# Kernel tuning notes

Measured on AMD Instinct MI355X. Metric: run time of the kernel, lower is better.

The kernel has to match this reference:

```python
import jax, jax.numpy as jnp
import numpy as np
from jax import lax

DIM = 1024
INNER = 2048  # dim * expand_factor
STATE = 64
B, T = 4, 2048
DECAY = 0.95
INPUT_FACTOR = 0.05
LN_EPS = 1e-5


def setup_inputs() -> dict:
    key = jax.random.key(0)
    ks = jax.random.split(key, 8)
    s = 0.02  # small weight scale
    return {
        "x": jax.random.normal(ks[0], (B, T, DIM), jnp.float32),
        "W_in": jax.random.normal(ks[1], (2 * INNER, DIM), jnp.float32) * s,
        "conv_w": jax.random.normal(ks[2], (INNER, 1, 4), jnp.float32) * s,
        "conv_b": jax.random.normal(ks[3], (INNER,), jnp.float32) * s,
        "W_B": jax.random.normal(ks[4], (STATE, INNER), jnp.float32) * s,
        "W_C": jax.random.normal(ks[5], (INNER, STATE), jnp.float32) * s,
        "D_param": jax.random.normal(ks[6], (INNER,), jnp.float32) * s,
        "W_out": jax.random.normal(ks[7], (DIM, INNER), jnp.float32) * s,
        "ln_gamma": jnp.ones((DIM,), jnp.float32),
        "ln_beta": jnp.zeros((DIM,), jnp.float32),
    }


def _layernorm(x, g, b):
    mu = jnp.mean(x, axis=-1, keepdims=True)
    var = jnp.mean(jnp.square(x - mu), axis=-1, keepdims=True)
    return (x - mu) * lax.rsqrt(var + LN_EPS) * g + b


def reference(x, W_in, conv_w, conv_b, W_B, W_C, D_param, W_out, ln_gamma, ln_beta):
    Bn, Tn, Dn = x.shape
    # in_proj -> split into input/gate halves
    x_proj = jnp.einsum("btd,ed->bte", x, W_in)  # [B,T,2*INNER]
    x_input, x_gate = jnp.split(x_proj, 2, axis=-1)
    # depthwise causal conv1d (torch pad=3 then slice [:T] == left-pad 3)
    xc = lax.conv_general_dilated(
        x_input.transpose(0, 2, 1),  # [B,C,T]
        conv_w,                       # [C,1,4]
        window_strides=(1,),
        padding=[(3, 0)],
        feature_group_count=INNER,
    ) + conv_b[None, :, None]
    u = jax.nn.silu(xc).transpose(0, 2, 1)  # [B,T,INNER]
    # linear recurrence: h_t = 0.95*h_{t-1} + 0.05*B_proj(u_t); h_0 = 0
    Bu = jnp.einsum("btc,sc->bts", u, W_B)  # [B,T,STATE]

    def step(h, bu_t):
        h = DECAY * h + INPUT_FACTOR * bu_t
        return h, h

    h0 = jnp.zeros((Bn, STATE), x.dtype)
    _, hs = lax.scan(step, h0, Bu.transpose(1, 0, 2))  # hs: [T,B,STATE]
    hs = hs.transpose(1, 0, 2)  # [B,T,STATE]
    y = jnp.einsum("bts,cs->btc", hs, W_C) + D_param * u  # [B,T,INNER]
    y = y * jax.nn.silu(x_gate)
    y = jnp.einsum("btc,dc->btd", y, W_out)  # [B,T,DIM]
    return _layernorm(y + x, ln_gamma, ln_beta)
```

## Files before the change

kernel.cpp:

```cpp
#include <hip/hip_runtime.h>
#include <hip/hip_bf16.h>

#define T_SEQ 2048
#define DIMD  1024
#define INNER 2048
#define STATE 64
#define BATCH 4
#define NCHUNK 64
#define CHUNK_L (T_SEQ / NCHUNK)
#define MROWS (BATCH * T_SEQ)
#define PSTRIDE ((long)MROWS * STATE)

typedef __hip_bfloat16 bf16;
typedef __attribute__((ext_vector_type(8))) short bf16x8v;
typedef __attribute__((ext_vector_type(4))) float f32x4v;
typedef __attribute__((ext_vector_type(4))) short short4v;

__device__ __forceinline__ float b2f(short s) {
    unsigned u = ((unsigned)(unsigned short)s) << 16;
    float f;
    __builtin_memcpy(&f, &u, 4);
    return f;
}
__device__ __forceinline__ short f2b(float f) {
    bf16 h = __float2bfloat16(f);
    short s;
    __builtin_memcpy(&s, &h, 2);
    return s;
}

__device__ __forceinline__ void gld_lds16(void* lds, const void* gsrc) {
    __builtin_amdgcn_global_load_lds(
        (const __attribute__((address_space(1))) unsigned*)gsrc,
        (__attribute__((address_space(3))) unsigned*)lds, 16, 0, 0);
}

template<int N> __device__ __forceinline__ void waitcnt_vm() {
    if constexpr (N == 8)       asm volatile("s_waitcnt vmcnt(8)" ::: "memory");
    else if constexpr (N == 4)  asm volatile("s_waitcnt vmcnt(4)" ::: "memory");
    else if constexpr (N == 2)  asm volatile("s_waitcnt vmcnt(2)" ::: "memory");
    else                        asm volatile("s_waitcnt vmcnt(0)" ::: "memory");
}
__device__ __forceinline__ void block_barrier() {
    asm volatile("" ::: "memory");
    __builtin_amdgcn_s_barrier();
    asm volatile("" ::: "memory");
}

template<int XSWZ>
__device__ __forceinline__ void swz_block(int& bx, int& by) {
    if constexpr (XSWZ == 1) {
        const int gx = gridDim.x;
        const int nwg = gx * gridDim.y;
        int id = by * gx + bx;
        const int cpx = nwg >> 3;
        id = (id & 7) * cpx + (id >> 3);
        bx = id % gx; by = id / gx;
    } else if constexpr (XSWZ == 2) {
        const int gx = gridDim.x;
        const int gy = gridDim.y;
        const int id = by * gx + bx;
        const int xcd = id & 7;
        const int c   = id >> 3;
        const int rowsX = gy >> 3;
        const int rw  = gx >> 2;
        const int r   = c >> 4;
        const int pos = c & 15;
        const int rbx = (r % rw) << 2;
        const int rby = (r / rw) << 2;
        bx = rbx + (pos & 3);
        by = xcd * rowsX + rby + (pos >> 2);
    }
}

template<int EPI, int XSWZ>
__global__ __launch_bounds__(512, 2)
void gemm_8ph(const short* __restrict__ A, const short* __restrict__ B,
              void* __restrict__ Cout, int M, int N, int K)
{
    __shared__ __align__(16) short As[2][2][128 * 64];
    __shared__ __align__(16) short Bs[2][2][128 * 64];

    int bx = blockIdx.x, by = blockIdx.y;
    swz_block<XSWZ>(bx, by);

    const int tid  = threadIdx.x;
    const int lane = tid & 63;
    const int wave = tid >> 6;
    const int wm2 = (wave >> 2) & 1;
    const int wn2 = wave & 3;
    const long bm = (long)by * 256;
    const long bn = (long)bx * 256;

    const int rsel = lane & 15;
    const int ssrc = (((tid & 7) ^ ((tid >> 3) & 7)) * 8);
    const int swz  = lane & 7;

    f32x4v acc[4][4][2];
#pragma unroll
    for (int q = 0; q < 4; q++)
#pragma unroll
        for (int m = 0; m < 4; m++)
#pragma unroll
            for (int n = 0; n < 2; n++)
                acc[q][m][n] = (f32x4v){0.f, 0.f, 0.f, 0.f};

    const int nt = K / 64;

    auto stage_half = [&](int tt, int h) {
        const int buf = tt & 1;
        const int half = h >> 1;
        const int k0 = tt * 64;
#pragma unroll
        for (int i = 0; i < 2; i++) {
            const int j = i * 512 + tid;
            if (h & 1)
                gld_lds16(&Bs[buf][half][j * 8],
                          &B[(bn + half * 128 + (j >> 3)) * (long)K + k0 + ssrc]);
            else
                gld_lds16(&As[buf][half][j * 8],
                          &A[(bm + half * 128 + (j >> 3)) * (long)K + k0 + ssrc]);
        }
    };

    stage_half(0, 0); stage_half(0, 1); stage_half(0, 2); stage_half(0, 3);
    waitcnt_vm<4>();
    block_barrier();

    for (int t = 0; t < nt; ++t) {
        const int buf = t & 1;
        const bool pf = (t + 1 < nt);
#pragma unroll
        for (int h = 0; h < 4; ++h) {
            const int QM[4] = {0, 1, 1, 0};
            const int QN[4] = {0, 0, 1, 1};
            const int qm = QM[h], qn = QN[h];
            bf16x8v af[4][2], bfv[2][2];
#pragma unroll
            for (int kkh = 0; kkh < 2; kkh++) {
                const int slog = kkh * 4 + (lane >> 4);
                const int soff = ((slog ^ swz) * 8);
#pragma unroll
                for (int m = 0; m < 4; m++) {
                    const int ar = wm2 * 64 + m * 16 + rsel;
                    af[m][kkh] = *(const bf16x8v*)&As[buf][qm][ar * 64 + soff];
                }
#pragma unroll
                for (int n = 0; n < 2; n++) {
                    const int br = wn2 * 32 + n * 16 + rsel;
                    bfv[n][kkh] = *(const bf16x8v*)&Bs[buf][qn][br * 64 + soff];
                }
            }
            if (pf) stage_half(t + 1, h);
            if (pf) {
                if (h == 0) waitcnt_vm<4>();
                else if (h == 1) waitcnt_vm<4>();
                else if (h == 3) waitcnt_vm<4>();
            } else {
                if (h == 0) waitcnt_vm<2>();
                else if (h == 1) waitcnt_vm<0>();
            }
            block_barrier();
            asm volatile("s_waitcnt lgkmcnt(0)" ::: "memory");
            __builtin_amdgcn_sched_barrier(0);
            __builtin_amdgcn_s_setprio(1);
#pragma unroll
            for (int kkh = 0; kkh < 2; kkh++)
#pragma unroll
                for (int m = 0; m < 4; m++)
#pragma unroll
                    for (int n = 0; n < 2; n++)
                        acc[h][m][n] = __builtin_amdgcn_mfma_f32_16x16x32_bf16(
                            af[m][kkh], bfv[n][kkh], acc[h][m][n], 0, 0, 0);
            __builtin_amdgcn_s_setprio(0);
            block_barrier();
        }
    }

#pragma unroll
    for (int q = 0; q < 4; q++) {
        const int QM[4] = {0, 1, 1, 0};
        const int QN[4] = {0, 0, 1, 1};
#pragma unroll
        for (int m = 0; m < 4; m++) {
#pragma unroll
            for (int n = 0; n < 2; n++) {
                const long col  = bn + QN[q] * 128 + wn2 * 32 + n * 16 + (lane & 15);
                const long row0 = bm + QM[q] * 128 + wm2 * 64 + m * 16 + (lane >> 4) * 4;
#pragma unroll
                for (int j = 0; j < 4; j++) {
                    const long idx = (row0 + j) * (long)N + col;
                    ((short*)Cout)[idx] = f2b(acc[q][m][n][j]);
                }
            }
        }
    }
}

template<int BM, int BN, int BK, int WR, int WC, int EPI, int SPLITK, int XSWZ>
__global__ __launch_bounds__(WR*WC*64, 2)
void gemm_ring(const short* __restrict__ A, const short* __restrict__ B,
               void* __restrict__ Cout, int M, int N, int K,
               const short* __restrict__ u_ptr)
{
    constexpr int MFR = BM / (WR * 16);
    constexpr int NFR = BN / (WC * 16);
    constexpr int THREADS = WR * WC * 64;
    constexpr int UPR = BK / 8;
    constexpr int AISS = (BM * UPR) / THREADS;
    constexpr int BISS = (BN * UPR) / THREADS;
    constexpr int LPS  = AISS + BISS;
    __shared__ __align__(16) short As[2][BM * BK];
    __shared__ __align__(16) short Bs[2][BN * BK];

    int bx = blockIdx.x, by = blockIdx.y;
    swz_block<XSWZ>(bx, by);

    const int tid  = threadIdx.x;
    const int lane = tid & 63;
    const int wave = tid >> 6;
    const int wm = (wave / WC) * (MFR * 16);
    const int wn = (wave % WC) * (NFR * 16);
    const long bm = (long)by * BM;
    const long bn = (long)bx * BN;

    f32x4v acc[MFR][NFR];
#pragma unroll
    for (int m = 0; m < MFR; m++)
#pragma unroll
        for (int n = 0; n < NFR; n++)
            acc[m][n] = (f32x4v){0.f, 0.f, 0.f, 0.f};

    const int rsel = lane & 15;
    const int ssrc = (((tid & 7) ^ ((tid >> 3) & 7)) * 8);
    const int swz  = lane & 7;

    int kbeg = 0, kend = K;
    if constexpr (SPLITK > 1) {
        const int kch = K / SPLITK;
        kbeg = blockIdx.z * kch;
        kend = kbeg + kch;
    }
    const int nt = (kend - kbeg) / BK;

    auto stage = [&](int buf, int k0) {
#pragma unroll
        for (int i = 0; i < AISS; i++) {
            const int j = i * THREADS + tid;
            gld_lds16(&As[buf][j * 8],
                      &A[(bm + (j >> 3)) * (long)K + k0 + ssrc]);
        }
#pragma unroll
        for (int i = 0; i < BISS; i++) {
            const int j = i * THREADS + tid;
            gld_lds16(&Bs[buf][j * 8],
                      &B[(bn + (j >> 3)) * (long)K + k0 + ssrc]);
        }
    };
    auto compute = [&](int buf) {
#pragma unroll
        for (int kk = 0; kk < BK; kk += 32) {
            const int slog = (kk >> 3) + (lane >> 4);
            const int soff = ((slog ^ swz) * 8);
            bf16x8v af[MFR], bfv[NFR];
#pragma unroll
            for (int m = 0; m < MFR; m++)
                af[m] = *(const bf16x8v*)&As[buf][(wm + m * 16 + rsel) * BK + soff];
#pragma unroll
            for (int n = 0; n < NFR; n++)
                bfv[n] = *(const bf16x8v*)&Bs[buf][(wn + n * 16 + rsel) * BK + soff];
#pragma unroll
            for (int m = 0; m < MFR; m++)
#pragma unroll
                for (int n = 0; n < NFR; n++)
                    acc[m][n] = __builtin_amdgcn_mfma_f32_16x16x32_bf16(
                        af[m], bfv[n], acc[m][n], 0, 0, 0);
        }
    };

    stage(0, kbeg);
    for (int t = 0; t < nt; ++t) {
        const bool pf = (t + 1 < nt);
        if (pf) stage((t + 1) & 1, kbeg + (t + 1) * BK);
        if (pf) waitcnt_vm<LPS>();
        else    waitcnt_vm<0>();
        block_barrier();
        compute(t & 1);
        block_barrier();
    }

    float* fout = (float*)Cout;
    if constexpr (SPLITK > 1)
        fout += (long)blockIdx.z * (long)M * N;

#pragma unroll
    for (int m = 0; m < MFR; m++) {
#pragma unroll
        for (int n = 0; n < NFR; n++) {
            const long col  = bn + wn + n * 16 + (lane & 15);
            const long row0 = bm + wm + m * 16 + (lane >> 4) * 4;
#pragma unroll
            for (int j = 0; j < 4; j++) {
                const long row = row0 + j;
                const float v = acc[m][n][j];
                const long idx = row * (long)N + col;
                if constexpr (EPI == 0) {
                    ((short*)Cout)[idx] = f2b(v);
                } else if constexpr (EPI == 1) {
                    fout[idx] = v;
                } else {
                    ((short*)Cout)[idx] = f2b(v + b2f(u_ptr[idx]));
                }
            }
        }
    }
}

__global__ __launch_bounds__(256)
void conv_silu_kernel(const short* __restrict__ xproj, const float* __restrict__ cw,
                      const float* __restrict__ cb, short* __restrict__ u)
{
    const int bt = blockIdx.x;
    const int t  = bt & (T_SEQ - 1);
    const int c0 = threadIdx.x * 8;

    float wreg[4][8];
#pragma unroll
    for (int i = 0; i < 8; i++) {
        float4 wv = *(const float4*)&cw[(c0 + i) * 4];
        wreg[0][i] = wv.x; wreg[1][i] = wv.y; wreg[2][i] = wv.z; wreg[3][i] = wv.w;
    }
    float acc[8];
#pragma unroll
    for (int i = 0; i < 8; i++) acc[i] = cb[c0 + i];

#pragma unroll
    for (int k = 0; k < 4; k++) {
        if (t - 3 + k < 0) continue;
        bf16x8v v = *(const bf16x8v*)&xproj[(long)(bt - 3 + k) * (2 * INNER) + c0];
#pragma unroll
        for (int i = 0; i < 8; i++) acc[i] += b2f(v[i]) * wreg[k][i];
    }
    short o[8];
#pragma unroll
    for (int i = 0; i < 8; i++) {
        float s = acc[i] / (1.f + __expf(-acc[i]));
        o[i] = f2b(s);
    }
    *(bf16x8v*)&u[(long)bt * INNER + c0] = *(const bf16x8v*)o;
}

#define EBS 132
__global__ __launch_bounds__(256, 2)
void gemm3_fused(const short* __restrict__ hs, const short* __restrict__ Wc,
                 short* __restrict__ yg, const short* __restrict__ gate_ptr,
                 const float* __restrict__ Dp)
{
    __shared__ __align__(16) short As[128 * 64];
    __shared__ __align__(16) short Bs[128 * 64];
    __shared__ __align__(16) float eb[64 * EBS];

    const int tid  = threadIdx.x;
    const int lane = tid & 63;
    const int wave = tid >> 6;
    const int wm = (wave >> 1) * 64;
    const int wn = (wave & 1) * 64;
    const long bm = (long)blockIdx.y * 128;
    const long bn = (long)blockIdx.x * 128;

    const int rsel = lane & 15;
    const int ssrc = (((tid & 7) ^ ((tid >> 3) & 7)) * 8);
    const int swz  = lane & 7;

#pragma unroll
    for (int i = 0; i < 4; i++) {
        const int j = i * 256 + tid;
        gld_lds16(&As[j * 8], &hs[(bm + (j >> 3)) * (long)STATE + ssrc]);
    }
#pragma unroll
    for (int i = 0; i < 4; i++) {
        const int j = i * 256 + tid;
        gld_lds16(&Bs[j * 8], &Wc[(bn + (j >> 3)) * (long)STATE + ssrc]);
    }
    waitcnt_vm<0>();
    block_barrier();

    f32x4v acc[4][4];
#pragma unroll
    for (int m = 0; m < 4; m++)
#pragma unroll
        for (int n = 0; n < 4; n++)
            acc[m][n] = (f32x4v){0.f, 0.f, 0.f, 0.f};

#pragma unroll
    for (int kk = 0; kk < 64; kk += 32) {
        const int slog = (kk >> 3) + (lane >> 4);
        const int soff = ((slog ^ swz) * 8);
        bf16x8v af[4], bfv[4];
#pragma unroll
        for (int m = 0; m < 4; m++)
            af[m] = *(const bf16x8v*)&As[(wm + m * 16 + rsel) * 64 + soff];
#pragma unroll
        for (int n = 0; n < 4; n++)
            bfv[n] = *(const bf16x8v*)&Bs[(wn + n * 16 + rsel) * 64 + soff];
#pragma unroll
        for (int m = 0; m < 4; m++)
#pragma unroll
            for (int n = 0; n < 4; n++)
                acc[m][n] = __builtin_amdgcn_mfma_f32_16x16x32_bf16(
                    af[m], bfv[n], acc[m][n], 0, 0, 0);
    }

#pragma unroll
    for (int p = 0; p < 2; p++) {
        block_barrier();
        if ((wm >> 6) == p) {
#pragma unroll
            for (int m = 0; m < 4; m++) {
#pragma unroll
                for (int n = 0; n < 4; n++) {
                    const int cl = wn + n * 16 + (lane & 15);
#pragma unroll
                    for (int j = 0; j < 4; j++) {
                        const int rl = m * 16 + (lane >> 4) * 4 + j;
                        eb[rl * EBS + cl] = acc[m][n][j];
                    }
                }
            }
        }
        block_barrier();
#pragma unroll
        for (int k = 0; k < 4; k++) {
            const int unit = k * 256 + tid;
            const int rl = unit >> 4, cg = (unit & 15) * 8;
            const long grow = bm + p * 64 + rl;
            const long gcol = bn + cg;
            f32x4v y0 = *(const f32x4v*)&eb[rl * EBS + cg];
            f32x4v y1 = *(const f32x4v*)&eb[rl * EBS + cg + 4];
            bf16x8v uv = *(const bf16x8v*)&yg[grow * (long)INNER + gcol];
            bf16x8v gv = *(const bf16x8v*)&gate_ptr[grow * (long)(2 * INNER) + gcol];
            short o[8];
#pragma unroll
            for (int i = 0; i < 8; i++) {
                const float yy = (i < 4 ? y0[i] : y1[i - 4]);
                const float uu = b2f(uv[i]);
                const float gg = b2f(gv[i]);
                const float yv = yy + Dp[gcol + i] * uu;
                const float sg = gg / (1.f + __expf(-gg));
                o[i] = f2b(yv * sg);
            }
            *(bf16x8v*)&yg[grow * (long)INNER + gcol] = *(const bf16x8v*)o;
        }
    }
}

__global__ __launch_bounds__(64)
void scan_local_kernel(const float* __restrict__ Bu, float* __restrict__ locfin)
{
    const int b  = blockIdx.x / NCHUNK;
    const int ch = blockIdx.x % NCHUNK;
    const long base = ((long)b * T_SEQ + (long)ch * CHUNK_L) * STATE + threadIdx.x;
    float h = 0.f;
#pragma unroll
    for (int t = 0; t < CHUNK_L; t++) {
        const long o = base + (long)t * STATE;
        float bu = (Bu[o] + Bu[o + PSTRIDE]) + (Bu[o + 2 * PSTRIDE] + Bu[o + 3 * PSTRIDE]);
        h = 0.95f * h + 0.05f * bu;
    }
    locfin[(long)blockIdx.x * STATE + threadIdx.x] = h;
}

__global__ __launch_bounds__(256)
void carry_kernel(const float* __restrict__ locfin, float* __restrict__ carry,
                  float decayL)
{
    __shared__ float sm[BATCH * NCHUNK * STATE];
    for (int i = threadIdx.x; i < BATCH * NCHUNK * STATE; i += 256)
        sm[i] = locfin[i];
    __syncthreads();
    const int b = threadIdx.x >> 6, s = threadIdx.x & 63;
    float c = 0.f;
    for (int ch = 0; ch < NCHUNK; ch++) {
        const int idx = (b * NCHUNK + ch) * STATE + s;
        carry[idx] = c;
        c = decayL * c + sm[idx];
    }
}

__global__ __launch_bounds__(64)
void scan_apply_kernel(const float* __restrict__ Bu, const float* __restrict__ carry,
                       short* __restrict__ hs)
{
    const int b  = blockIdx.x / NCHUNK;
    const int ch = blockIdx.x % NCHUNK;
    const long base = ((long)b * T_SEQ + (long)ch * CHUNK_L) * STATE + threadIdx.x;
    float h = carry[(long)blockIdx.x * STATE + threadIdx.x];
#pragma unroll
    for (int t = 0; t < CHUNK_L; t++) {
        const long o = base + (long)t * STATE;
        float bu = (Bu[o] + Bu[o + PSTRIDE]) + (Bu[o + 2 * PSTRIDE] + Bu[o + 3 * PSTRIDE]);
        h = 0.95f * h + 0.05f * bu;
        hs[o] = f2b(h);
    }
}

__global__ __launch_bounds__(256)
void ln_kernel(const short* __restrict__ yx, const float* __restrict__ g,
               const float* __restrict__ b, float* __restrict__ out)
{
    const int row = blockIdx.x;
    const int c   = threadIdx.x * 4;
    const long off = (long)row * DIMD + c;
    const short4v yv = *(const short4v*)&yx[off];
    float s0 = b2f(yv[0]), s1 = b2f(yv[1]), s2 = b2f(yv[2]), s3 = b2f(yv[3]);
    float sum = s0 + s1 + s2 + s3;
    float sq  = s0 * s0 + s1 * s1 + s2 * s2 + s3 * s3;
#pragma unroll
    for (int o = 32; o > 0; o >>= 1) {
        sum += __shfl_down(sum, o);
        sq  += __shfl_down(sq, o);
    }
    __shared__ float rs[4], rq[4];
    const int wave = threadIdx.x >> 6, lane = threadIdx.x & 63;
    if (lane == 0) { rs[wave] = sum; rq[wave] = sq; }
    __syncthreads();
    float tsum = rs[0] + rs[1] + rs[2] + rs[3];
    float tsq  = rq[0] + rq[1] + rq[2] + rq[3];
    float mu  = tsum * (1.f / DIMD);
    float inv = rsqrtf(tsq * (1.f / DIMD) - mu * mu + 1e-5f);
    float4 gv = *(const float4*)&g[c];
    float4 bv = *(const float4*)&b[c];
    float4 ov;
    ov.x = (s0 - mu) * inv * gv.x + bv.x;
    ov.y = (s1 - mu) * inv * gv.y + bv.y;
    ov.z = (s2 - mu) * inv * gv.z + bv.z;
    ov.w = (s3 - mu) * inv * gv.w + bv.w;
    *(float4*)&out[off] = ov;
}

#define C4_X   2097152L
#define C4_W1  (C4_X + 1048576L)
#define C4_WB  (C4_W1 + 32768L)
#define C4_WC  (C4_WB + 32768L)
#define C4_TOT (C4_WC + 524288L)

__global__ __launch_bounds__(256)
void cvt5_kernel(const float* __restrict__ x, const float* __restrict__ w1,
                 const float* __restrict__ wB, const float* __restrict__ wC,
                 const float* __restrict__ wO, short* __restrict__ dst)
{
    const long i = (long)blockIdx.x * 256 + threadIdx.x;
    if (i >= C4_TOT) return;
    const float* s;
    long off;
    if      (i < C4_X)  { s = x;  off = i; }
    else if (i < C4_W1) { s = w1; off = i - C4_X; }
    else if (i < C4_WB) { s = wB; off = i - C4_W1; }
    else if (i < C4_WC) { s = wC; off = i - C4_WB; }
    else                { s = wO; off = i - C4_WC; }
    float4 v = *(const float4*)&s[off * 4];
    short4v o = { f2b(v.x), f2b(v.y), f2b(v.z), f2b(v.w) };
    *(short4v*)&dst[i * 4] = o;
}

extern "C" void kernel_launch(void* const* d_in, const int* in_sizes, int n_in,
                              void* d_out, int out_size, void* d_ws, size_t ws_size,
                              hipStream_t stream)
{
    const float* x     = (const float*)d_in[0];
    const float* W_in  = (const float*)d_in[1];
    const float* cw    = (const float*)d_in[2];
    const float* cb    = (const float*)d_in[3];
    const float* W_B   = (const float*)d_in[4];
    const float* W_C   = (const float*)d_in[5];
    const float* Dp    = (const float*)d_in[6];
    const float* W_out = (const float*)d_in[7];
    const float* ln_g  = (const float*)d_in[8];
    const float* ln_b  = (const float*)d_in[9];

    char* p = (char*)d_ws;
    short* xw    = (short*)(p);
    short* w1    = (short*)(p +  16777216);
    short* wB    = (short*)(p +  25165824);
    short* wC    = (short*)(p +  25427968);
    short* wO    = (short*)(p +  25690112);
    short* xproj = (short*)(p +  29884416);
    short* u     = (short*)(p +  96993280);
    short* hs    = (short*)(p + 132644864);
    short* yg    = u;
    short* yx    = xproj;
    float* BuP    = (float*)(p + 16777216);
    float* locfin = (float*)(p + 25165824);
    float* carry  = (float*)(p + 25231360);

    const int M = MROWS;

    cvt5_kernel<<<(int)((C4_TOT + 255) / 256), 256, 0, stream>>>(
        x, W_in, W_B, W_C, W_out, xw);

    gemm_8ph<0, 2><<<dim3(2 * INNER / 256, M / 256), 512, 0, stream>>>(
        xw, w1, xproj, M, 2 * INNER, DIMD);

    conv_silu_kernel<<<M, 256, 0, stream>>>(xproj, cw, cb, u);

    gemm_ring<64, 64, 64, 2, 2, 1, 4, 0><<<dim3(1, M / 64, 4), 256, 0, stream>>>(
        u, wB, BuP, M, STATE, INNER, nullptr);

    float decayL;
    {
        double dd = 1.0;
        for (int i = 0; i < CHUNK_L; i++) dd *= 0.95;
        decayL = (float)dd;
    }
    scan_local_kernel<<<BATCH * NCHUNK, STATE, 0, stream>>>(BuP, locfin);
    carry_kernel<<<1, 256, 0, stream>>>(locfin, carry, decayL);
    scan_apply_kernel<<<BATCH * NCHUNK, STATE, 0, stream>>>(BuP, carry, hs);

    gemm3_fused<<<dim3(INNER / 128, M / 128), 256, 0, stream>>>(
        hs, wC, yg, xproj + INNER, Dp);

    gemm_ring<128, 128, 64, 2, 2, 3, 1, 1><<<dim3(DIMD / 128, M / 128), 256, 0, stream>>>(
        yg, wO, yx, M, DIMD, INNER, xw);

    ln_kernel<<<M, 256, 0, stream>>>(yx, ln_g, ln_b, (float*)d_out);
}
```

Baseline: 249.7 us.

## Merge carry scan into scan_apply and cut one barrier per GEMM phase

The in_proj GEMM main loop now waits on outstanding loads and does one block barrier at the start of each quarter-phase, instead of a wait plus two barriers around the MFMA block. Separately, the single-block carry kernel is removed: each scan_apply block recomputes its own chunk carry by serially folding the earlier chunk finals. This saves one kernel launch and one serial single-block pass, at the cost of redundant per-block carry work (up to 63 steps). The barrier change reduces synchronization overhead but relies on the new wait counts being correct for the double-buffered LDS reuse.

```diff
diff --git a/kernel.cpp b/kernel.cpp
--- a/kernel.cpp
+++ b/kernel.cpp
@@ -124,14 +124,21 @@
     };
 
     stage_half(0, 0); stage_half(0, 1); stage_half(0, 2); stage_half(0, 3);
-    waitcnt_vm<4>();
-    block_barrier();
 
     for (int t = 0; t < nt; ++t) {
         const int buf = t & 1;
         const bool pf = (t + 1 < nt);
 #pragma unroll
         for (int h = 0; h < 4; ++h) {
+            if (pf) {
+                if (h < 3) waitcnt_vm<4>();
+            } else {
+                if (h == 0) waitcnt_vm<4>();
+                else if (h == 1) waitcnt_vm<2>();
+                else if (h == 2) waitcnt_vm<0>();
+            }
+            block_barrier();
+
             const int QM[4] = {0, 1, 1, 0};
             const int QN[4] = {0, 0, 1, 1};
             const int qm = QM[h], qn = QN[h];
@@ -152,15 +159,7 @@
                 }
             }
             if (pf) stage_half(t + 1, h);
-            if (pf) {
-                if (h == 0) waitcnt_vm<4>();
-                else if (h == 1) waitcnt_vm<4>();
-                else if (h == 3) waitcnt_vm<4>();
-            } else {
-                if (h == 0) waitcnt_vm<2>();
-                else if (h == 1) waitcnt_vm<0>();
-            }
-            block_barrier();
+
             asm volatile("s_waitcnt lgkmcnt(0)" ::: "memory");
             __builtin_amdgcn_sched_barrier(0);
             __builtin_amdgcn_s_setprio(1);
@@ -173,7 +172,6 @@
                         acc[h][m][n] = __builtin_amdgcn_mfma_f32_16x16x32_bf16(
                             af[m][kkh], bfv[n][kkh], acc[h][m][n], 0, 0, 0);
             __builtin_amdgcn_s_setprio(0);
-            block_barrier();
         }
     }
 
@@ -470,31 +468,16 @@
     locfin[(long)blockIdx.x * STATE + threadIdx.x] = h;
 }
 
-__global__ __launch_bounds__(256)
-void carry_kernel(const float* __restrict__ locfin, float* __restrict__ carry,
-                  float decayL)
-{
-    __shared__ float sm[BATCH * NCHUNK * STATE];
-    for (int i = threadIdx.x; i < BATCH * NCHUNK * STATE; i += 256)
-        sm[i] = locfin[i];
-    __syncthreads();
-    const int b = threadIdx.x >> 6, s = threadIdx.x & 63;
-    float c = 0.f;
-    for (int ch = 0; ch < NCHUNK; ch++) {
-        const int idx = (b * NCHUNK + ch) * STATE + s;
-        carry[idx] = c;
-        c = decayL * c + sm[idx];
-    }
-}
-
 __global__ __launch_bounds__(64)
-void scan_apply_kernel(const float* __restrict__ Bu, const float* __restrict__ carry,
-                       short* __restrict__ hs)
+void scan_apply_kernel(const float* __restrict__ Bu, const float* __restrict__ locfin,
+                       short* __restrict__ hs, float decayL)
 {
     const int b  = blockIdx.x / NCHUNK;
     const int ch = blockIdx.x % NCHUNK;
+    float h = 0.f;
+    for (int j = 0; j < ch; j++)
+        h = decayL * h + locfin[((long)b * NCHUNK + j) * STATE + threadIdx.x];
     const long base = ((long)b * T_SEQ + (long)ch * CHUNK_L) * STATE + threadIdx.x;
-    float h = carry[(long)blockIdx.x * STATE + threadIdx.x];
 #pragma unroll
     for (int t = 0; t < CHUNK_L; t++) {
         const long o = base + (long)t * STATE;
@@ -591,7 +574,6 @@
     short* yx    = xproj;
     float* BuP    = (float*)(p + 16777216);
     float* locfin = (float*)(p + 25165824);
-    float* carry  = (float*)(p + 25231360);
 
     const int M = MROWS;
 
@@ -613,8 +595,7 @@
         decayL = (float)dd;
     }
     scan_local_kernel<<<BATCH * NCHUNK, STATE, 0, stream>>>(BuP, locfin);
-    carry_kernel<<<1, 256, 0, stream>>>(locfin, carry, decayL);
-    scan_apply_kernel<<<BATCH * NCHUNK, STATE, 0, stream>>>(BuP, carry, hs);
+    scan_apply_kernel<<<BATCH * NCHUNK, STATE, 0, stream>>>(BuP, locfin, hs, decayL);
 
     gemm3_fused<<<dim3(INNER / 128, M / 128), 256, 0, stream>>>(
         hs, wC, yg, xproj + INNER, Dp);
```

Result: no change. 251.5 us (+0.7%).

## Double-buffer LDS fragment reads across quadrants to overlap with MFMA

Applied to the files above, without the earlier changes.

Restructures the 256x256 GEMM main loop so the LDS fragment reads for the next quadrant are issued into alternating register sets while the current quadrant's MFMAs run. Partial lgkmcnt waits replace the full lgkmcnt(0), and the barriers and global prefetch waits are reordered, with the next tile's first quadrant read at the end of each iteration. The aim is to hide LDS latency and cut barrier stalls, at the cost of doubling the fragment registers, which may reduce occupancy or cause spills. It also depends on fine-grained hand-counted waits being correct.

```diff
diff --git a/kernel.cpp b/kernel.cpp
--- a/kernel.cpp
+++ b/kernel.cpp
@@ -40,6 +40,10 @@
     else if constexpr (N == 4)  asm volatile("s_waitcnt vmcnt(4)" ::: "memory");
     else if constexpr (N == 2)  asm volatile("s_waitcnt vmcnt(2)" ::: "memory");
     else                        asm volatile("s_waitcnt vmcnt(0)" ::: "memory");
+}
+template<int N> __device__ __forceinline__ void waitcnt_lgkm() {
+    if constexpr (N == 12)      asm volatile("s_waitcnt lgkmcnt(12)" ::: "memory");
+    else                        asm volatile("s_waitcnt lgkmcnt(0)" ::: "memory");
 }
 __device__ __forceinline__ void block_barrier() {
     asm volatile("" ::: "memory");
@@ -96,6 +100,9 @@
     const int ssrc = (((tid & 7) ^ ((tid >> 3) & 7)) * 8);
     const int swz  = lane & 7;
 
+    const int QM4[4] = {0, 1, 1, 0};
+    const int QN4[4] = {0, 0, 1, 1};
+
     f32x4v acc[4][4][2];
 #pragma unroll
     for (int q = 0; q < 4; q++)
@@ -123,70 +130,90 @@
         }
     };
 
+    bf16x8v afE[4][2], bfE[2][2], afO[4][2], bfO[2][2];
+
+    auto rd = [&](int rbuf, int q, bf16x8v (&Af)[4][2], bf16x8v (&Bf)[2][2]) {
+        const int qm = QM4[q], qn = QN4[q];
+#pragma unroll
+        for (int kkh = 0; kkh < 2; kkh++) {
+            const int slog = kkh * 4 + (lane >> 4);
+            const int soff = ((slog ^ swz) * 8);
+#pragma unroll
+            for (int m = 0; m < 4; m++) {
+                const int ar = wm2 * 64 + m * 16 + rsel;
+                Af[m][kkh] = *(const bf16x8v*)&As[rbuf][qm][ar * 64 + soff];
+            }
+#pragma unroll
+            for (int n = 0; n < 2; n++) {
+                const int br = wn2 * 32 + n * 16 + rsel;
+                Bf[n][kkh] = *(const bf16x8v*)&Bs[rbuf][qn][br * 64 + soff];
+            }
+        }
+    };
+    auto mm = [&](int q, bf16x8v (&Af)[4][2], bf16x8v (&Bf)[2][2]) {
+        __builtin_amdgcn_s_setprio(1);
+#pragma unroll
+        for (int kkh = 0; kkh < 2; kkh++)
+#pragma unroll
+            for (int m = 0; m < 4; m++)
+#pragma unroll
+                for (int n = 0; n < 2; n++)
+                    acc[q][m][n] = __builtin_amdgcn_mfma_f32_16x16x32_bf16(
+                        Af[m][kkh], Bf[n][kkh], acc[q][m][n], 0, 0, 0);
+        __builtin_amdgcn_s_setprio(0);
+    };
+
     stage_half(0, 0); stage_half(0, 1); stage_half(0, 2); stage_half(0, 3);
     waitcnt_vm<4>();
     block_barrier();
+    rd(0, 0, afE, bfE);
 
     for (int t = 0; t < nt; ++t) {
         const int buf = t & 1;
         const bool pf = (t + 1 < nt);
-#pragma unroll
-        for (int h = 0; h < 4; ++h) {
-            const int QM[4] = {0, 1, 1, 0};
-            const int QN[4] = {0, 0, 1, 1};
-            const int qm = QM[h], qn = QN[h];
-            bf16x8v af[4][2], bfv[2][2];
-#pragma unroll
-            for (int kkh = 0; kkh < 2; kkh++) {
-                const int slog = kkh * 4 + (lane >> 4);
-                const int soff = ((slog ^ swz) * 8);
-#pragma unroll
-                for (int m = 0; m < 4; m++) {
-                    const int ar = wm2 * 64 + m * 16 + rsel;
-                    af[m][kkh] = *(const bf16x8v*)&As[buf][qm][ar * 64 + soff];
-                }
-#pragma unroll
-                for (int n = 0; n < 2; n++) {
-                    const int br = wn2 * 32 + n * 16 + rsel;
-                    bfv[n][kkh] = *(const bf16x8v*)&Bs[buf][qn][br * 64 + soff];
-                }
-            }
-            if (pf) stage_half(t + 1, h);
-            if (pf) {
-                if (h == 0) waitcnt_vm<4>();
-                else if (h == 1) waitcnt_vm<4>();
-                else if (h == 3) waitcnt_vm<4>();
-            } else {
-                if (h == 0) waitcnt_vm<2>();
-                else if (h == 1) waitcnt_vm<0>();
-            }
+        waitcnt_vm<2>();
+        block_barrier();
+        rd(buf, 1, afO, bfO);
+        if (pf) stage_half(t + 1, 0);
+        waitcnt_lgkm<12>();
+        __builtin_amdgcn_sched_barrier(0);
+        mm(0, afE, bfE);
+        if (pf) waitcnt_vm<2>();
+        else    waitcnt_vm<0>();
+        block_barrier();
+        rd(buf, 2, afE, bfE);
+        if (pf) stage_half(t + 1, 1);
+        waitcnt_lgkm<12>();
+        __builtin_amdgcn_sched_barrier(0);
+        mm(1, afO, bfO);
+        rd(buf, 3, afO, bfO);
+        if (pf) stage_half(t + 1, 2);
+        waitcnt_lgkm<12>();
+        __builtin_amdgcn_sched_barrier(0);
+        mm(2, afE, bfE);
+        if (pf) {
+            waitcnt_vm<2>();
             block_barrier();
-            asm volatile("s_waitcnt lgkmcnt(0)" ::: "memory");
+            rd(buf ^ 1, 0, afE, bfE);
+            stage_half(t + 1, 3);
+            waitcnt_lgkm<12>();
             __builtin_amdgcn_sched_barrier(0);
-            __builtin_amdgcn_s_setprio(1);
-#pragma unroll
-            for (int kkh = 0; kkh < 2; kkh++)
-#pragma unroll
-                for (int m = 0; m < 4; m++)
-#pragma unroll
-                    for (int n = 0; n < 2; n++)
-                        acc[h][m][n] = __builtin_amdgcn_mfma_f32_16x16x32_bf16(
-                            af[m][kkh], bfv[n][kkh], acc[h][m][n], 0, 0, 0);
-            __builtin_amdgcn_s_setprio(0);
-            block_barrier();
+            mm(3, afO, bfO);
+        } else {
+            waitcnt_lgkm<0>();
+            __builtin_amdgcn_sched_barrier(0);
+            mm(3, afO, bfO);
         }
     }
 
 #pragma unroll
     for (int q = 0; q < 4; q++) {
-        const int QM[4] = {0, 1, 1, 0};
-        const int QN[4] = {0, 0, 1, 1};
 #pragma unroll
         for (int m = 0; m < 4; m++) {
 #pragma unroll
             for (int n = 0; n < 2; n++) {
-                const long col  = bn + QN[q] * 128 + wn2 * 32 + n * 16 + (lane & 15);
-                const long row0 = bm + QM[q] * 128 + wm2 * 64 + m * 16 + (lane >> 4) * 4;
+                const long col  = bn + QN4[q] * 128 + wn2 * 32 + n * 16 + (lane & 15);
+                const long row0 = bm + QM4[q] * 128 + wm2 * 64 + m * 16 + (lane >> 4) * 4;
 #pragma unroll
                 for (int j = 0; j < 4; j++) {
                     const long idx = (row0 + j) * (long)N + col;
```

Result: slower. 339.5 us (+35.9%).
